# Kernel optimization log

Hardware: AMD Instinct MI355X
Metric: run time of the kernel (lower is better)

The kernel has to match this reference:

```python
import jax, jax.numpy as jnp
import numpy as np

# NSA config (matches init_kwargs)
B, S, D = 1, 1024, 2048
H, G = 32, 2              # query heads, kv heads (GQA groups)
DQ, DV = 128, 128          # qk head dim, v head dim
BLOCK, TOPN, WINDOW = 64, 4, 256  # select/compress block, top-k blocks, sliding window
NEG = -1e30


def setup_inputs() -> dict:
    key = jax.random.key(0)
    ks = jax.random.split(key, 6)
    x = jax.random.normal(ks[0], (B, S, D), jnp.float32)
    Wq = jax.random.normal(ks[1], (D, H * DQ), jnp.float32) * 0.02
    Wk = jax.random.normal(ks[2], (D, G * DQ), jnp.float32) * 0.02
    Wv = jax.random.normal(ks[3], (D, G * DV), jnp.float32) * 0.02
    Wo = jax.random.normal(ks[4], (H * DV, D), jnp.float32) * 0.02
    Wc = jax.random.normal(ks[5], (D, H * 3), jnp.float32) * 0.02
    # standard RoPE tables, HF layout [B, S, head_dim]
    inv = 1.0 / (10000.0 ** (jnp.arange(0, DQ, 2, dtype=jnp.float32) / DQ))
    ang = jnp.arange(S, dtype=jnp.float32)[:, None] * inv[None, :]
    emb = jnp.concatenate([ang, ang], axis=-1)
    return dict(hidden_states=x, cos=jnp.cos(emb)[None], sin=jnp.sin(emb)[None],
                Wq=Wq, Wk=Wk, Wv=Wv, Wo=Wo, Wc=Wc)


def _rope(t, cos, sin):
    # t: [B,S,N,Dh]; rotate_half RoPE
    half = t.shape[-1] // 2
    rot = jnp.concatenate([-t[..., half:], t[..., :half]], axis=-1)
    return t * cos[:, :, None, :] + rot * sin[:, :, None, :]


def _nsa_forward(x, cos, sin, Wq, Wk, Wv, Wo, Wc):
    scale = 1.0 / np.sqrt(DQ).astype(np.float32)
    h = H // G                      # query heads per kv group
    C = S // BLOCK                  # number of blocks
    q = (x @ Wq).reshape(B, S, H, DQ)
    k = (x @ Wk).reshape(B, S, G, DQ)
    v = (x @ Wv).reshape(B, S, G, DV)
    gates = jax.nn.sigmoid((x @ Wc).reshape(B, S, H, 3))
    q = _rope(q, cos, sin)
    k = _rope(k, cos, sin)
    qg = q.reshape(B, S, G, h, DQ)
    s_idx = jnp.arange(S)
    c_idx = jnp.arange(C)

    # ---- branch 1: compressed attention (mean-pooled blocks) ----
    kb = k.reshape(B, C, BLOCK, G, DQ)
    vb = v.reshape(B, C, BLOCK, G, DV)
    kc = kb.mean(2)  # [B,C,G,DQ]
    vc = vb.mean(2)  # [B,C,G,DV]
    lc = jnp.einsum('bsghd,bcgd->bsghc', qg, kc) * scale
    # block fully in the past: block end <= s
    mc = ((c_idx + 1) * BLOCK - 1)[None, :] <= s_idx[:, None]  # [S,C]
    mcb = mc[None, :, None, None, :]
    pc = jax.nn.softmax(jnp.where(mcb, lc, NEG), axis=-1) * mcb  # zero rows with no visible block
    o_cmp = jnp.einsum('bsghc,bcgd->bsghd', pc, vc).reshape(B, S, H, DV)

    # ---- block selection (importance = compressed probs summed over group heads) ----
    imp = pc.sum(3)  # [B,S,G,C]
    valid = (c_idx[None, :] * BLOCK) <= s_idx[:, None]          # candidate blocks
    cur = s_idx // BLOCK
    force = (c_idx[None, :] == 0) | (c_idx[None, :] == cur[:, None])  # always keep first + current block
    imp = jnp.where((valid & force)[None, :, None, :], 1e9,
                    jnp.where(valid[None, :, None, :], imp, -1e9))
    _, idx = jax.lax.top_k(imp, TOPN)  # [B,S,G,TOPN]

    # ---- branch 2: selected-block attention (gather only top-k blocks) ----
    kb_t = kb.transpose(0, 3, 1, 2, 4)   # [B,G,C,BLOCK,DQ]
    vb_t = vb.transpose(0, 3, 1, 2, 4)
    idx_t = idx.transpose(0, 2, 1, 3)    # [B,G,S,TOPN]
    gather = jax.vmap(jax.vmap(lambda blocks, ix: blocks[ix]))
    ksel = gather(kb_t, idx_t)  # [B,G,S,n,BLOCK,DQ]
    vsel = gather(vb_t, idx_t)  # [B,G,S,n,BLOCK,DV]
    ls = jnp.einsum('bsghd,bgsnkd->bsghnk', qg, ksel) * scale
    pos = idx[..., None] * BLOCK + jnp.arange(BLOCK)  # token position of each selected slot [B,S,G,n,BLOCK]
    msel = (pos <= s_idx[None, :, None, None, None])[:, :, :, None, :, :]
    ls = jnp.where(msel, ls, NEG)
    shp = ls.shape
    ps = jax.nn.softmax(ls.reshape(*shp[:4], -1), axis=-1).reshape(shp)
    o_slc = jnp.einsum('bsghnk,bgsnkd->bsghd', ps, vsel).reshape(B, S, H, DV)

    # ---- branch 3: sliding-window causal attention ----
    lw = jnp.einsum('bsghd,btgd->bsght', qg, k) * scale
    mw = (s_idx[None, :] <= s_idx[:, None]) & (s_idx[None, :] > s_idx[:, None] - WINDOW)  # [S,T]
    pw = jax.nn.softmax(jnp.where(mw[None, :, None, None, :], lw, NEG), axis=-1)
    o_win = jnp.einsum('bsght,btgd->bsghd', pw, v).reshape(B, S, H, DV)

    # ---- gated combine + output projection ----
    o = gates[..., 0:1] * o_cmp + gates[..., 1:2] * o_slc + gates[..., 2:3] * o_win
    return o.reshape(B, S, H * DV) @ Wo


def reference(hidden_states, cos, sin, Wq, Wk, Wv, Wo, Wc):
    return _nsa_forward(hidden_states, cos, sin, Wq, Wk, Wv, Wo, Wc)
```

## Files before the change

kernel.cpp:

```cpp
#include <hip/hip_runtime.h>

#define S_LEN 1024
#define DMODEL 2048
#define NH 32
#define NG 2
#define HPG 16
#define DQK 128
#define NBLK 16
#define BLKSZ 64
#define TOPN 4
#define WIN 256
#define SCALE 0.08838834764831845f

typedef float f32x4 __attribute__((ext_vector_type(4)));
typedef __bf16 bf16x8 __attribute__((ext_vector_type(8)));

__device__ __forceinline__ unsigned short f2bf(float f){
    unsigned int u = __builtin_bit_cast(unsigned int, f);
    u += 0x7fffu + ((u >> 16) & 1u);
    return (unsigned short)(u >> 16);
}
__device__ __forceinline__ float bf2f(unsigned short h){
    unsigned int u = ((unsigned int)h) << 16;
    return __builtin_bit_cast(float, u);
}

using as1_u32 = __attribute__((address_space(1))) const unsigned int;
using as3_u32 = __attribute__((address_space(3))) unsigned int;
__device__ __forceinline__ void g2l16(const void* g, void* l){
    __builtin_amdgcn_global_load_lds((as1_u32*)g, (as3_u32*)l, 16, 0, 0);
}

__global__ __launch_bounds__(256) void split_convert(
    const float* __restrict__ in, unsigned short* __restrict__ hi,
    unsigned short* __restrict__ lo, int n)
{
    int i = blockIdx.x * 256 + threadIdx.x;
    if (i < n){
        float v = in[i];
        unsigned short h = f2bf(v);
        hi[i] = h;
        lo[i] = f2bf(v - bf2f(h));
    }
}

__global__ __launch_bounds__(1024) void transpose_split(
    const float* __restrict__ W, unsigned short* __restrict__ WT_hi,
    unsigned short* __restrict__ WT_lo, int K, int N)
{
    __shared__ float t[32][33];
    int tx = threadIdx.x, ty = threadIdx.y;
    int k0 = blockIdx.y * 32, n0 = blockIdx.x * 32;
    int nn = n0 + tx;
    float val = 0.f;
    if (nn < N) val = W[(size_t)(k0 + ty) * N + nn];
    t[ty][tx] = val;
    __syncthreads();
    int n2 = n0 + ty;
    if (n2 < N){
        float v2 = t[tx][ty];
        unsigned short h = f2bf(v2);
        WT_hi[(size_t)n2 * K + k0 + tx] = h;
        if (WT_lo){
            WT_lo[(size_t)n2 * K + k0 + tx] = f2bf(v2 - bf2f(h));
        }
    }
}

template<int NTERM, int MODE>
__global__ __launch_bounds__(256) void gemm_fused(
    const unsigned short* __restrict__ Ah, const unsigned short* __restrict__ Al,
    const unsigned short* __restrict__ Bh, const unsigned short* __restrict__ Bl,
    float* __restrict__ Co, int M, int N, int K)
{
    __shared__ __align__(16) unsigned short smem[NTERM == 3 ? 24576 : 12288];
    unsigned short* As_h = smem;
    unsigned short* Bs_h = smem + 8192;
    unsigned short* As_l = smem + 12288;
    unsigned short* Bs_l = smem + 20480;

    int gx = gridDim.x;
    int nwg = gx * gridDim.y;
    int bid = blockIdx.y * gx + blockIdx.x;
    int chunk = nwg >> 3;
    bid = (bid & 7) * chunk + (bid >> 3);
    const int n0 = (bid % gx) * 64;
    const int m0 = (bid / gx) * 128;

    const int kz = blockIdx.z;
    const int Kloc = K / gridDim.z;
    const int kbeg = kz * Kloc;
    Co += (size_t)kz * M * N;

    const int tid = threadIdx.x;
    const int lane = tid & 63;
    const int l15 = lane & 15;
    const int g4 = lane >> 4;
    const int w = tid >> 6;
    const int wr = w >> 1, wc = w & 1;
    const int ar = tid >> 3;
    const int ac = (tid & 7) * 8;

    f32x4 acc[4][2] = {};

    for (int k0 = kbeg; k0 < kbeg + Kloc; k0 += 64){
        #pragma unroll
        for (int p = 0; p < 4; p++){
            int r = p*32 + ar;
            size_t go = (size_t)(m0 + r) * K + k0 + ac;
            int lo_ = p*2048 + tid*8;
            g2l16(Ah + go, As_h + lo_);
            if constexpr (NTERM == 3) g2l16(Al + go, As_l + lo_);
        }
        #pragma unroll
        for (int p = 0; p < 2; p++){
            int r = p*32 + ar;
            int nr = n0 + r; if (nr > N - 1) nr = N - 1;
            size_t go = (size_t)nr * K + k0 + ac;
            int lo_ = p*2048 + tid*8;
            g2l16(Bh + go, Bs_h + lo_);
            if constexpr (NTERM == 3) g2l16(Bl + go, Bs_l + lo_);
        }
        __syncthreads();
        #pragma unroll
        for (int ks = 0; ks < 2; ks++){
            const int kc_ = ks*32 + g4*8;
            bf16x8 ah[4], bh[2], al[4], bl[2];
            #pragma unroll
            for (int mi = 0; mi < 4; mi++){
                int row = wr*64 + mi*16 + l15;
                ah[mi] = *(const bf16x8*)&As_h[row*64 + kc_];
                if constexpr (NTERM == 3) al[mi] = *(const bf16x8*)&As_l[row*64 + kc_];
            }
            #pragma unroll
            for (int ni = 0; ni < 2; ni++){
                int row = wc*32 + ni*16 + l15;
                bh[ni] = *(const bf16x8*)&Bs_h[row*64 + kc_];
                if constexpr (NTERM == 3) bl[ni] = *(const bf16x8*)&Bs_l[row*64 + kc_];
            }
            #pragma unroll
            for (int mi = 0; mi < 4; mi++)
                #pragma unroll
                for (int ni = 0; ni < 2; ni++){
                    acc[mi][ni] = __builtin_amdgcn_mfma_f32_16x16x32_bf16(
                        ah[mi], bh[ni], acc[mi][ni], 0, 0, 0);
                    if constexpr (NTERM == 3){
                        acc[mi][ni] = __builtin_amdgcn_mfma_f32_16x16x32_bf16(
                            ah[mi], bl[ni], acc[mi][ni], 0, 0, 0);
                        acc[mi][ni] = __builtin_amdgcn_mfma_f32_16x16x32_bf16(
                            al[mi], bh[ni], acc[mi][ni], 0, 0, 0);
                    }
                }
        }
        __syncthreads();
    }
    #pragma unroll
    for (int mi = 0; mi < 4; mi++)
        #pragma unroll
        for (int ni = 0; ni < 2; ni++){
            int col = n0 + wc*32 + ni*16 + l15;
            if (col < N){
                int rbase = m0 + wr*64 + mi*16 + g4*4;
                #pragma unroll
                for (int j = 0; j < 4; j++){
                    float v = acc[mi][ni][j];
                    if (MODE == 1) v = 1.f / (1.f + __expf(-v));
                    Co[(size_t)(rbase + j) * N + col] = v;
                }
            }
        }
}

__global__ __launch_bounds__(256) void reduce_kvg(
    const float* __restrict__ part, float* __restrict__ kbuf,
    float* __restrict__ vbuf, float* __restrict__ gbuf)
{
    int i = blockIdx.x * 256 + threadIdx.x;
    if (i >= 1024*608) return;
    int s = i / 608, c = i % 608;
    size_t o = (size_t)s * 640 + c;
    const size_t stride = 1024ull * 640;
    float sum = part[o] + part[o + stride] + part[o + 2*stride] + part[o + 3*stride];
    if (c < 256) kbuf[s*256 + c] = sum;
    else if (c < 512) vbuf[s*256 + (c - 256)] = sum;
    else gbuf[s*96 + (c - 512)] = 1.f / (1.f + __expf(-sum));
}

__global__ __launch_bounds__(256) void rope_kernel(
    float* __restrict__ t, const float* __restrict__ cosb,
    const float* __restrict__ sinb, int nh, int total)
{
    int i = blockIdx.x * 256 + threadIdx.x;
    if (i >= total) return;
    int d = i & 63;
    int r = i >> 6;
    int s = r / nh;
    size_t base = (size_t)r * 128;
    float lo_v = t[base + d], hi_v = t[base + 64 + d];
    float cl = cosb[s*128 + d],      sl = sinb[s*128 + d];
    float ch = cosb[s*128 + 64 + d], sh = sinb[s*128 + 64 + d];
    t[base + d]      = lo_v * cl - hi_v * sl;
    t[base + 64 + d] = hi_v * ch + lo_v * sh;
}

__global__ __launch_bounds__(256) void mean_blocks(
    const float* __restrict__ src, float* __restrict__ dst)
{
    int i = blockIdx.x * 256 + threadIdx.x;
    if (i >= NBLK * NG * DQK) return;
    int d = i & 127;
    int g = (i >> 7) & 1;
    int c = i >> 8;
    float s_ = 0.f;
    for (int j = 0; j < BLKSZ; j++)
        s_ += src[((size_t)(c*BLKSZ + j) * NG + g) * DQK + d];
    dst[i] = s_ * (1.f / 64.f);
}

__global__ __launch_bounds__(256) void kb_convert(
    const float* __restrict__ in, unsigned short* __restrict__ out, int n4)
{
    int i = blockIdx.x * 256 + threadIdx.x;
    if (i < n4){
        f32x4 v = ((const f32x4*)in)[i];
        ushort4 o;
        o.x = f2bf(v[0]); o.y = f2bf(v[1]); o.z = f2bf(v[2]); o.w = f2bf(v[3]);
        ((ushort4*)out)[i] = o;
    }
}

__global__ __launch_bounds__(1024) void vt_transpose(
    const float* __restrict__ v, unsigned short* __restrict__ Vt)
{
    __shared__ float t[32][33];
    int g = blockIdx.z;
    int s0 = blockIdx.x * 32, d0 = blockIdx.y * 32;
    int tx = threadIdx.x, ty = threadIdx.y;
    t[ty][tx] = v[((size_t)(s0 + ty)*NG + g)*DQK + d0 + tx];
    __syncthreads();
    Vt[((size_t)g*DQK + d0 + ty)*S_LEN + s0 + tx] = f2bf(t[tx][ty]);
}

__global__ __launch_bounds__(256) void cmp_attn(
    const float* __restrict__ q, const float* __restrict__ kc,
    const float* __restrict__ vc, const float* __restrict__ gates,
    float* __restrict__ o_acc, int* __restrict__ idxb)
{
    int s = blockIdx.x, g = blockIdx.y;
    __shared__ float qs[16][132];
    __shared__ float kcs[16][132];
    __shared__ float vcs[16][132];
    __shared__ float pcs[16][16];
    __shared__ float imps[16];
    int tid = threadIdx.x;
    for (int i = tid; i < 16*128; i += 256){
        int a = i >> 7, d = i & 127;
        qs[a][d]  = q[((size_t)s*NH + g*HPG + a)*DQK + d];
        kcs[a][d] = kc[((size_t)a*NG + g)*DQK + d];
        vcs[a][d] = vc[((size_t)a*NG + g)*DQK + d];
    }
    __syncthreads();
    int hh = tid >> 4, c = tid & 15;
    float acc = 0.f;
    for (int d4 = 0; d4 < 128; d4 += 4){
        f32x4 qv = *(const f32x4*)&qs[hh][d4];
        f32x4 kv = *(const f32x4*)&kcs[c][d4];
        acc += qv[0]*kv[0] + qv[1]*kv[1] + qv[2]*kv[2] + qv[3]*kv[3];
    }
    acc *= SCALE;
    bool vis = ((c + 1)*BLKSZ - 1) <= s;
    float l = vis ? acc : -1e30f;
    float m = l;
    #pragma unroll
    for (int off = 1; off < 16; off <<= 1) m = fmaxf(m, __shfl_xor(m, off));
    float p = vis ? __expf(l - m) : 0.f;
    float Z = p;
    #pragma unroll
    for (int off = 1; off < 16; off <<= 1) Z += __shfl_xor(Z, off);
    p = (Z > 0.f) ? (p / Z) : 0.f;
    pcs[hh][c] = p;
    __syncthreads();
    if (tid < 16){
        float si = 0.f;
        for (int a = 0; a < 16; a++) si += pcs[a][tid];
        imps[tid] = si;
    }
    __syncthreads();
    for (int i = tid; i < HPG*DQK; i += 256){
        int h2 = i >> 7, d = i & 127;
        float o = 0.f;
        #pragma unroll
        for (int cc = 0; cc < 16; cc++) o += pcs[h2][cc] * vcs[cc][d];
        int hf = g*HPG + h2;
        o_acc[((size_t)s*NH + hf)*DQK + d] = gates[((size_t)s*NH + hf)*3 + 0] * o;
    }
    if (tid == 0){
        int cur = s >> 6;
        float sc[16];
        #pragma unroll
        for (int c2 = 0; c2 < 16; c2++){
            bool valid = (c2*BLKSZ) <= s;
            bool force = (c2 == 0) || (c2 == cur);
            sc[c2] = (valid && force) ? 1e9f : (valid ? imps[c2] : -1e9f);
        }
        int base = (s*NG + g)*TOPN;
        #pragma unroll
        for (int n = 0; n < TOPN; n++){
            float bv = -1e38f; int bi = 0;
            for (int c2 = 0; c2 < 16; c2++) if (sc[c2] > bv){ bv = sc[c2]; bi = c2; }
            idxb[base + n] = bi;
            sc[bi] = -1e38f;
        }
    }
}

__global__ __launch_bounds__(256) void fused_attn(
    const float* __restrict__ q,
    const unsigned short* __restrict__ Kb,
    const unsigned short* __restrict__ Vt,
    const float* __restrict__ gates,
    const int* __restrict__ idxb,
    const float* __restrict__ o_acc,
    unsigned short* __restrict__ ob)
{
    const int s = blockIdx.x, g = blockIdx.y;
    const int tid = threadIdx.x;
    const int w = tid >> 6;
    const int lane = tid & 63;
    const int l15 = lane & 15;
    const int g4 = lane >> 4;
    __shared__ __align__(16) unsigned short K_lds[64*128];
    __shared__ __align__(16) unsigned short V_lds[128*64];
    __shared__ __align__(16) unsigned short P_lds[16][336];
    __shared__ float redm[4][16];
    __shared__ float reds[4][16];
    __shared__ int bidx[4];
    if (tid < 4) bidx[tid] = idxb[(s*NG + g)*TOPN + tid];

    bf16x8 qf[4];
    {
        const float* qrow = &q[((size_t)s*NH + g*HPG + l15)*DQK];
        #pragma unroll
        for (int ks = 0; ks < 4; ks++){
            int d0 = ks*32 + g4*8;
            f32x4 a = *(const f32x4*)(qrow + d0);
            f32x4 b = *(const f32x4*)(qrow + d0 + 4);
            bf16x8 r;
            #pragma unroll
            for (int i = 0; i < 4; i++){
                r[i]     = __builtin_bit_cast(__bf16, f2bf(a[i]));
                r[i + 4] = __builtin_bit_cast(__bf16, f2bf(b[i]));
            }
            qf[ks] = r;
        }
    }
    int wbase = (s >= 255) ? ((s - 255) & ~63) : 0;
    if (wbase > S_LEN - 320) wbase = S_LEN - 320;
    f32x4 oacc[2] = {};
    __syncthreads();

    #pragma unroll
    for (int br = 0; br < 2; br++){
        const int nch = (br == 0) ? 4 : 5;
        float sv[20];
        float mymax = -1e30f;
        for (int c = 0; c < nch; c++){
            int keybase = (br == 0) ? bidx[c]*64 : (wbase + c*64);
            #pragma unroll
            for (int p = 0; p < 4; p++){
                int row = p*16 + (tid >> 4);
                int colb = ((tid & 15) << 4) ^ ((row & 7) << 4);
                const char* src = (const char*)Kb + (size_t)((keybase + row)*2 + g)*256 + colb;
                g2l16(src, (char*)K_lds + p*4096 + tid*16);
            }
            __syncthreads();
            f32x4 acc = {};
            {
                int r = w*16 + l15;
                const char* kb_ = (const char*)K_lds + r*256;
                int swz = (r & 7) << 4;
                #pragma unroll
                for (int ks2 = 0; ks2 < 4; ks2++){
                    bf16x8 kf = *(const bf16x8*)(kb_ + ((ks2*64 + g4*16) ^ swz));
                    acc = __builtin_amdgcn_mfma_f32_16x16x32_bf16(kf, qf[ks2], acc, 0, 0, 0);
                }
            }
            __syncthreads();
            #pragma unroll
            for (int j = 0; j < 4; j++){
                int pos = keybase + w*16 + g4*4 + j;
                float v = acc[j] * SCALE;
                bool ok = (pos <= s) && (br == 0 || pos + WIN > s);
                sv[c*4 + j] = ok ? v : -1e30f;
                mymax = fmaxf(mymax, sv[c*4 + j]);
            }
        }
        {
            int keybase = (br == 0) ? bidx[0]*64 : wbase;
            #pragma unroll
            for (int p = 0; p < 4; p++){
                int row = p*32 + (tid >> 3);
                int colb = ((tid & 7) << 4) ^ ((row & 7) << 4);
                const char* src = (const char*)Vt + ((size_t)(g*128 + row)*S_LEN + keybase)*2 + colb;
                g2l16(src, (char*)V_lds + p*4096 + tid*16);
            }
        }
        mymax = fmaxf(mymax, __shfl_xor(mymax, 16));
        mymax = fmaxf(mymax, __shfl_xor(mymax, 32));
        if (lane < 16) redm[w][lane] = mymax;
        __syncthreads();
        float gm = fmaxf(fmaxf(redm[0][l15], redm[1][l15]),
                         fmaxf(redm[2][l15], redm[3][l15]));
        float mysum = 0.f;
        #pragma unroll
        for (int c = 0; c < 5; c++) if (c < nch)
            #pragma unroll
            for (int j = 0; j < 4; j++){
                float e = (sv[c*4 + j] > -1e29f) ? __expf(sv[c*4 + j] - gm) : 0.f;
                sv[c*4 + j] = e;
                mysum += e;
            }
        mysum += __shfl_xor(mysum, 16);
        mysum += __shfl_xor(mysum, 32);
        if (lane < 16) reds[w][lane] = mysum;
        __syncthreads();
        float Z = reds[0][l15] + reds[1][l15] + reds[2][l15] + reds[3][l15];
        float gate = gates[((size_t)s*NH + g*HPG + l15)*3 + 1 + br];
        float fac = gate / Z;
        #pragma unroll
        for (int c = 0; c < 5; c++) if (c < nch)
            #pragma unroll
            for (int jp = 0; jp < 2; jp++){
                int key = c*64 + w*16 + g4*4 + jp*2;
                unsigned int pk = (unsigned int)f2bf(sv[c*4 + jp*2] * fac)
                                | ((unsigned int)f2bf(sv[c*4 + jp*2 + 1] * fac) << 16);
                *(unsigned int*)&P_lds[l15][key] = pk;
            }
        __syncthreads();
        for (int c = 0; c < nch; c++){
            #pragma unroll
            for (int sub = 0; sub < 2; sub++){
                bf16x8 pf = *(const bf16x8*)&P_lds[l15][c*64 + sub*32 + g4*8];
                #pragma unroll
                for (int dt = 0; dt < 2; dt++){
                    int row = (2*w + dt)*16 + l15;
                    const char* vb = (const char*)V_lds + row*128
                                   + ((sub*64 + g4*16) ^ ((row & 7) << 4));
                    bf16x8 vf = *(const bf16x8*)vb;
                    oacc[dt] = __builtin_amdgcn_mfma_f32_16x16x32_bf16(pf, vf, oacc[dt], 0, 0, 0);
                }
            }
            __syncthreads();
            if (c + 1 < nch){
                int keybase = (br == 0) ? bidx[c+1]*64 : (wbase + (c+1)*64);
                #pragma unroll
                for (int p = 0; p < 4; p++){
                    int row = p*32 + (tid >> 3);
                    int colb = ((tid & 7) << 4) ^ ((row & 7) << 4);
                    const char* src = (const char*)Vt + ((size_t)(g*128 + row)*S_LEN + keybase)*2 + colb;
                    g2l16(src, (char*)V_lds + p*4096 + tid*16);
                }
                __syncthreads();
            }
        }
        __syncthreads();
    }
    #pragma unroll
    for (int dt = 0; dt < 2; dt++){
        int d = (2*w + dt)*16 + l15;
        #pragma unroll
        for (int j = 0; j < 4; j++){
            int h = g4*4 + j;
            size_t oo = ((size_t)s*NH + g*HPG + h)*DQK + d;
            ob[oo] = f2bf(o_acc[oo] + oacc[dt][j]);
        }
    }
}

extern "C" void kernel_launch(void* const* d_in, const int* in_sizes, int n_in,
                              void* d_out, int out_size, void* d_ws, size_t ws_size,
                              hipStream_t stream)
{
    (void)in_sizes; (void)n_in; (void)out_size; (void)ws_size;
    const float* x    = (const float*)d_in[0];
    const float* cosb = (const float*)d_in[1];
    const float* sinb = (const float*)d_in[2];
    const float* Wq   = (const float*)d_in[3];
    const float* Wk   = (const float*)d_in[4];
    const float* Wv   = (const float*)d_in[5];
    const float* Wo   = (const float*)d_in[6];
    const float* Wc   = (const float*)d_in[7];
    float* out = (float*)d_out;

    char* ws = (char*)d_ws;
    size_t off = 0;
    auto alloc = [&](size_t bytes)->char*{
        char* p = ws + off;
        off += (bytes + 255) & ~(size_t)255;
        return p;
    };
    unsigned short* WqT_hi = (unsigned short*)alloc(4096ull*2048*2);
    unsigned short* WqT_lo = (unsigned short*)alloc(4096ull*2048*2);
    unsigned short* xb_hi  = (unsigned short*)alloc(1024ull*2048*2);
    unsigned short* xb_lo  = (unsigned short*)alloc(1024ull*2048*2);
    unsigned short* BcT_hi = (unsigned short*)alloc(640ull*2048*2);
    unsigned short* BcT_lo = (unsigned short*)alloc(640ull*2048*2);
    float* qbuf  = (float*)alloc(1024ull*32*128*4);
    float* kbuf  = (float*)alloc(1024ull*2*128*4);
    float* vbuf  = (float*)alloc(1024ull*2*128*4);
    float* gbuf  = (float*)alloc(1024ull*96*4);
    float* kcb   = (float*)alloc(16ull*2*128*4);
    float* vcb   = (float*)alloc(16ull*2*128*4);
    int*   idxb  = (int*)alloc(1024ull*2*4*4);
    float* partials = (float*)WqT_hi;
    float* o_acc = (float*)WqT_hi;
    unsigned short* WoT = WqT_lo;
    unsigned short* ob  = xb_hi;
    unsigned short* Kbb = BcT_hi;
    unsigned short* Vt  = BcT_lo;

    split_convert<<<dim3((1024*2048)/256), 256, 0, stream>>>(x, xb_hi, xb_lo, 1024*2048);
    transpose_split<<<dim3(128, 64), dim3(32,32), 0, stream>>>(Wq, WqT_hi, WqT_lo, 2048, 4096);
    transpose_split<<<dim3(8, 64), dim3(32,32), 0, stream>>>(Wk, BcT_hi, BcT_lo, 2048, 256);
    transpose_split<<<dim3(8, 64), dim3(32,32), 0, stream>>>(Wv, BcT_hi + 256ull*2048, BcT_lo + 256ull*2048, 2048, 256);
    transpose_split<<<dim3(3, 64), dim3(32,32), 0, stream>>>(Wc, BcT_hi + 512ull*2048, BcT_lo + 512ull*2048, 2048, 96);
    gemm_fused<3,0><<<dim3(64,8), 256, 0, stream>>>(xb_hi, xb_lo, WqT_hi, WqT_lo, qbuf, 1024, 4096, 2048);
    gemm_fused<3,0><<<dim3(10,8,4), 256, 0, stream>>>(xb_hi, xb_lo, BcT_hi, BcT_lo, partials, 1024, 640, 2048);
    reduce_kvg<<<dim3(2432), 256, 0, stream>>>(partials, kbuf, vbuf, gbuf);
    transpose_split<<<dim3(64, 128), dim3(32,32), 0, stream>>>(Wo, WoT, nullptr, 4096, 2048);
    rope_kernel<<<dim3((1024*32*64)/256), 256, 0, stream>>>(qbuf, cosb, sinb, 32, 1024*32*64);
    rope_kernel<<<dim3((1024*2*64)/256), 256, 0, stream>>>(kbuf, cosb, sinb, 2, 1024*2*64);
    mean_blocks<<<dim3(16), 256, 0, stream>>>(kbuf, kcb);
    mean_blocks<<<dim3(16), 256, 0, stream>>>(vbuf, vcb);
    kb_convert<<<dim3((1024*2*128/4 + 255)/256), 256, 0, stream>>>(kbuf, Kbb, 1024*2*128/4);
    vt_transpose<<<dim3(1024/32, 128/32, 2), dim3(32,32), 0, stream>>>(vbuf, Vt);
    cmp_attn<<<dim3(1024,2), 256, 0, stream>>>(qbuf, kcb, vcb, gbuf, o_acc, idxb);
    fused_attn<<<dim3(1024,2), 256, 0, stream>>>(qbuf, Kbb, Vt, gbuf, idxb, o_acc, ob);
    gemm_fused<1,0><<<dim3(32,8), 256, 0, stream>>>(ob, nullptr, WoT, nullptr, out, 1024, 2048, 4096);
}
```

Baseline: 387.0 us.

## Swizzle GEMM LDS, split-K output projection, fuse rope/convert and mean kernels

Applies an XOR swizzle to the GEMM's LDS tile layout by permuting global source columns and read offsets, aiming to reduce LDS bank conflicts. The output projection is split along K into two partial slabs that a new vectorized kernel sums, which gives twice as many workgroups at the cost of extra memory traffic. The K RoPE is fused with bf16 conversion, the two block-mean launches are merged into one, and the P_lds row pitch is padded differently. Together these cut kernel launch count and the GEMM's shared-memory stalls.

```diff
diff --git a/kernel.cpp b/kernel.cpp
--- a/kernel.cpp
+++ b/kernel.cpp
@@ -100,6 +100,8 @@
     const int wr = w >> 1, wc = w & 1;
     const int ar = tid >> 3;
     const int ac = (tid & 7) * 8;
+    const int acs = ac ^ ((ar & 7) << 3);
+    const int rswz = (l15 & 7) << 3;
 
     f32x4 acc[4][2] = {};
 
@@ -107,7 +109,7 @@
         #pragma unroll
         for (int p = 0; p < 4; p++){
             int r = p*32 + ar;
-            size_t go = (size_t)(m0 + r) * K + k0 + ac;
+            size_t go = (size_t)(m0 + r) * K + k0 + acs;
             int lo_ = p*2048 + tid*8;
             g2l16(Ah + go, As_h + lo_);
             if constexpr (NTERM == 3) g2l16(Al + go, As_l + lo_);
@@ -116,7 +118,7 @@
         for (int p = 0; p < 2; p++){
             int r = p*32 + ar;
             int nr = n0 + r; if (nr > N - 1) nr = N - 1;
-            size_t go = (size_t)nr * K + k0 + ac;
+            size_t go = (size_t)nr * K + k0 + acs;
             int lo_ = p*2048 + tid*8;
             g2l16(Bh + go, Bs_h + lo_);
             if constexpr (NTERM == 3) g2l16(Bl + go, Bs_l + lo_);
@@ -124,7 +126,7 @@
         __syncthreads();
         #pragma unroll
         for (int ks = 0; ks < 2; ks++){
-            const int kc_ = ks*32 + g4*8;
+            const int kc_ = (ks*32 + g4*8) ^ rswz;
             bf16x8 ah[4], bh[2], al[4], bl[2];
             #pragma unroll
             for (int mi = 0; mi < 4; mi++){
@@ -186,6 +188,15 @@
     else gbuf[s*96 + (c - 512)] = 1.f / (1.f + __expf(-sum));
 }
 
+__global__ __launch_bounds__(256) void reduce_out(
+    const float* __restrict__ part, float* __restrict__ out)
+{
+    int i = blockIdx.x * 256 + threadIdx.x;
+    f32x4 a = ((const f32x4*)part)[i];
+    f32x4 b = ((const f32x4*)part)[i + 524288];
+    ((f32x4*)out)[i] = a + b;
+}
+
 __global__ __launch_bounds__(256) void rope_kernel(
     float* __restrict__ t, const float* __restrict__ cosb,
     const float* __restrict__ sinb, int nh, int total)
@@ -203,30 +214,43 @@
     t[base + 64 + d] = hi_v * ch + lo_v * sh;
 }
 
-__global__ __launch_bounds__(256) void mean_blocks(
-    const float* __restrict__ src, float* __restrict__ dst)
+__global__ __launch_bounds__(256) void rope_k_kernel(
+    float* __restrict__ t, const float* __restrict__ cosb,
+    const float* __restrict__ sinb, unsigned short* __restrict__ kb)
 {
     int i = blockIdx.x * 256 + threadIdx.x;
-    if (i >= NBLK * NG * DQK) return;
-    int d = i & 127;
-    int g = (i >> 7) & 1;
-    int c = i >> 8;
+    if (i >= 1024*2*64) return;
+    int d = i & 63;
+    int r = i >> 6;
+    int s = r >> 1;
+    size_t base = (size_t)r * 128;
+    float lo_v = t[base + d], hi_v = t[base + 64 + d];
+    float cl = cosb[s*128 + d],      sl = sinb[s*128 + d];
+    float ch = cosb[s*128 + 64 + d], sh = sinb[s*128 + 64 + d];
+    float nl = lo_v * cl - hi_v * sl;
+    float nh = hi_v * ch + lo_v * sh;
+    t[base + d]      = nl;
+    t[base + 64 + d] = nh;
+    kb[base + d]      = f2bf(nl);
+    kb[base + 64 + d] = f2bf(nh);
+}
+
+__global__ __launch_bounds__(256) void mean_blocks2(
+    const float* __restrict__ ksrc, const float* __restrict__ vsrc,
+    float* __restrict__ kc, float* __restrict__ vc)
+{
+    int i = blockIdx.x * 256 + threadIdx.x;
+    if (i >= 2*NBLK*NG*DQK) return;
+    const float* src = (i < NBLK*NG*DQK) ? ksrc : vsrc;
+    float* dst = (i < NBLK*NG*DQK) ? kc : vc;
+    int j = i & (NBLK*NG*DQK - 1);
+    int d = j & 127;
+    int g = (j >> 7) & 1;
+    int c = j >> 8;
     float s_ = 0.f;
-    for (int j = 0; j < BLKSZ; j++)
-        s_ += src[((size_t)(c*BLKSZ + j) * NG + g) * DQK + d];
-    dst[i] = s_ * (1.f / 64.f);
-}
-
-__global__ __launch_bounds__(256) void kb_convert(
-    const float* __restrict__ in, unsigned short* __restrict__ out, int n4)
-{
-    int i = blockIdx.x * 256 + threadIdx.x;
-    if (i < n4){
-        f32x4 v = ((const f32x4*)in)[i];
-        ushort4 o;
-        o.x = f2bf(v[0]); o.y = f2bf(v[1]); o.z = f2bf(v[2]); o.w = f2bf(v[3]);
-        ((ushort4*)out)[i] = o;
-    }
+    for (int jj = 0; jj < BLKSZ; jj++)
+        s_ += src[((size_t)(c*BLKSZ + jj) * NG + g) * DQK + d];
+    dst[j] = s_ * (1.f / 64.f);
 }
 
 __global__ __launch_bounds__(1024) void vt_transpose(
@@ -331,7 +355,7 @@
     const int g4 = lane >> 4;
     __shared__ __align__(16) unsigned short K_lds[64*128];
     __shared__ __align__(16) unsigned short V_lds[128*64];
-    __shared__ __align__(16) unsigned short P_lds[16][336];
+    __shared__ __align__(16) unsigned short P_lds[16][340];
     __shared__ float redm[4][16];
     __shared__ float reds[4][16];
     __shared__ int bidx[4];
@@ -514,6 +538,7 @@
     int*   idxb  = (int*)alloc(1024ull*2*4*4);
     float* partials = (float*)WqT_hi;
     float* o_acc = (float*)WqT_hi;
+    float* wo_part = (float*)WqT_hi;
     unsigned short* WoT = WqT_lo;
     unsigned short* ob  = xb_hi;
     unsigned short* Kbb = BcT_hi;
@@ -529,12 +554,11 @@
     reduce_kvg<<<dim3(2432), 256, 0, stream>>>(partials, kbuf, vbuf, gbuf);
     transpose_split<<<dim3(64, 128), dim3(32,32), 0, stream>>>(Wo, WoT, nullptr, 4096, 2048);
     rope_kernel<<<dim3((1024*32*64)/256), 256, 0, stream>>>(qbuf, cosb, sinb, 32, 1024*32*64);
-    rope_kernel<<<dim3((1024*2*64)/256), 256, 0, stream>>>(kbuf, cosb, sinb, 2, 1024*2*64);
-    mean_blocks<<<dim3(16), 256, 0, stream>>>(kbuf, kcb);
-    mean_blocks<<<dim3(16), 256, 0, stream>>>(vbuf, vcb);
-    kb_convert<<<dim3((1024*2*128/4 + 255)/256), 256, 0, stream>>>(kbuf, Kbb, 1024*2*128/4);
+    rope_k_kernel<<<dim3((1024*2*64)/256), 256, 0, stream>>>(kbuf, cosb, sinb, Kbb);
+    mean_blocks2<<<dim3(32), 256, 0, stream>>>(kbuf, vbuf, kcb, vcb);
     vt_transpose<<<dim3(1024/32, 128/32, 2), dim3(32,32), 0, stream>>>(vbuf, Vt);
     cmp_attn<<<dim3(1024,2), 256, 0, stream>>>(qbuf, kcb, vcb, gbuf, o_acc, idxb);
     fused_attn<<<dim3(1024,2), 256, 0, stream>>>(qbuf, Kbb, Vt, gbuf, idxb, o_acc, ob);
-    gemm_fused<1,0><<<dim3(32,8), 256, 0, stream>>>(ob, nullptr, WoT, nullptr, out, 1024, 2048, 4096);
-}
+    gemm_fused<1,0><<<dim3(32,8,2), 256, 0, stream>>>(ob, nullptr, WoT, nullptr, wo_part, 1024, 2048, 4096);
+    reduce_out<<<dim3(2048), 256, 0, stream>>>(wo_part, out);
+}
```

Result: faster. 344.2 us (-11.1%).
